# Kernel tuning notes

Measured on AMD Instinct MI355X. Metric: run time of the kernel, lower is better.

## Reference

```python
import jax, jax.numpy as jnp
import numpy as np

NUM_HEAD = 8  # matches init_kwargs num_head


def setup_inputs() -> dict:
    key = jax.random.key(0)
    ks = jax.random.split(key, 8)
    B, N, C, P = 2, 1024, 512, 256
    cluster_num = 8
    s = 0.02
    return {
        "x_token": jax.random.normal(ks[0], (B, N, C), jnp.float32),
        "x_path": jax.random.normal(ks[1], (B, N, P), jnp.float32),
        "idx_cluster": jax.random.randint(ks[2], (B, N), 0, cluster_num),
        "cluster_num": cluster_num,
        "Wq": jax.random.normal(ks[3], (C, C), jnp.float32) * s,
        "Wk": jax.random.normal(ks[4], (C, C), jnp.float32) * s,
        "Wv": jax.random.normal(ks[5], (C, C), jnp.float32) * s,
        "Wproj": jax.random.normal(ks[6], (C, C), jnp.float32) * s,
        "bproj": jnp.zeros((C,), jnp.float32),
    }


def reference(x_token, x_path, idx_cluster, cluster_num, Wq, Wk, Wv, Wproj, bproj):
    eps = 1e-6
    B, N, C = x_token.shape
    H = NUM_HEAD
    hd = C // H
    scale = hd ** -0.5

    # Linear projections (torch Linear: y = x @ W^T), qkv_bias=False
    q = x_token @ Wq.T
    k = x_token @ Wk.T
    v = (x_token @ Wv.T).reshape(B, N, H, hd).transpose(0, 2, 1, 3)  # (B,H,N,hd)

    qh = q.reshape(B, N, H, hd).transpose(0, 2, 1, 3)  # (B,H,N,hd)
    kh = k.reshape(B, N, H, hd).transpose(0, 2, 1, 3)

    # Raw scaled scores, computed once instead of per-cluster scatter/repeat
    s_ = jnp.einsum('bhid,bhjd->bhij', qh, kh) * scale  # (B,H,N,N)

    # One-hot cluster membership: (B, cluster_num, N)
    m = (idx_cluster[:, None, :] == jnp.arange(cluster_num)[None, :, None]).astype(s_.dtype)

    # attn_map[b,c,h,i,j] = s_[b,h,i,j] if idx[b,i]==c and idx[b,j]==c else 0
    attn_map = s_[:, None] * m[:, :, None, :, None] * m[:, :, None, None, :]  # (B,K,H,N,N)

    # Sum over clusters -> within-cluster scores, zeros elsewhere
    attn = attn_map.sum(axis=1)  # (B,H,N,N)

    # Custom eps-smoothed exp normalization (masked_fill on exact zeros, as in source)
    attn = jnp.where(attn == 0, jnp.float32(-1e9), attn).astype(jnp.float32)
    attn = jnp.exp(attn)
    attn = (attn + eps / N) / (attn.sum(axis=-1, keepdims=True) + eps)

    out = jnp.einsum('bhij,bhjd->bhid', attn, v)  # (B,H,N,hd)
    out = out.transpose(0, 2, 1, 3).reshape(B, N, C)
    out = out @ Wproj.T + bproj
    return out, attn_map
```

## Files before the change

### kernel.cpp

```cpp
#include <hip/hip_runtime.h>
#include <hip/hip_bf16.h>
#include <cstdint>
#include <cstddef>

#define NB   2
#define NN   1024
#define NC   512
#define NH   8
#define NHD  64
#define NK   8

typedef __attribute__((ext_vector_type(8))) short short8v;
typedef __attribute__((ext_vector_type(4))) short short4v;
typedef __attribute__((ext_vector_type(4))) float f32x4;

__device__ __forceinline__ short f2bf(float f) {
    union { float f; unsigned u; } v; v.f = f;
    unsigned r = v.u + 0x7FFFu + ((v.u >> 16) & 1u);
    return (short)(r >> 16);
}
__device__ __forceinline__ float bf2f(short s) {
    union { unsigned u; float f; } v;
    v.u = ((unsigned)(unsigned short)s) << 16;
    return v.f;
}
__device__ __forceinline__ short8v cvt8(const float* p) {
    float4 a = *(const float4*)p;
    float4 b = *(const float4*)(p + 4);
    short8v r;
    r[0] = f2bf(a.x); r[1] = f2bf(a.y); r[2] = f2bf(a.z); r[3] = f2bf(a.w);
    r[4] = f2bf(b.x); r[5] = f2bf(b.y); r[6] = f2bf(b.z); r[7] = f2bf(b.w);
    return r;
}

__global__ __launch_bounds__(256) void qkv_kernel(
    const float* __restrict__ x, const float* __restrict__ wq,
    const float* __restrict__ wk, const float* __restrict__ wv,
    short* __restrict__ qb, short* __restrict__ kb, short* __restrict__ vT) {
    __shared__ short As[64][40];
    __shared__ short Bs[64][40];
    const int tid = threadIdx.x;
    const int z = blockIdx.z;
    const float* Bsrc = (z == 0) ? wq : ((z == 1) ? wk : wv);
    const int m0 = blockIdx.y * 64, n0 = blockIdx.x * 64;
    const int lane = tid & 63, wave = tid >> 6;
    const int wm = wave >> 1, wn = wave & 1, quad = lane >> 4, lr = lane & 15;
    const int row = tid >> 2, c0 = (tid & 3) * 8;
    f32x4 acc[2][2] = {};
    for (int kt = 0; kt < 512; kt += 32) {
        *(short8v*)&As[row][c0] = cvt8(x + (m0 + row) * 512 + kt + c0);
        *(short8v*)&Bs[row][c0] = cvt8(Bsrc + (n0 + row) * 512 + kt + c0);
        __syncthreads();
        short8v a0 = *(short8v*)&As[wm * 32 + lr][quad * 8];
        short8v a1 = *(short8v*)&As[wm * 32 + 16 + lr][quad * 8];
        short8v b0 = *(short8v*)&Bs[wn * 32 + lr][quad * 8];
        short8v b1 = *(short8v*)&Bs[wn * 32 + 16 + lr][quad * 8];
        acc[0][0] = __builtin_amdgcn_mfma_f32_16x16x32_bf16(a0, b0, acc[0][0], 0, 0, 0);
        acc[0][1] = __builtin_amdgcn_mfma_f32_16x16x32_bf16(a0, b1, acc[0][1], 0, 0, 0);
        acc[1][0] = __builtin_amdgcn_mfma_f32_16x16x32_bf16(a1, b0, acc[1][0], 0, 0, 0);
        acc[1][1] = __builtin_amdgcn_mfma_f32_16x16x32_bf16(a1, b1, acc[1][1], 0, 0, 0);
        __syncthreads();
    }
    for (int sm = 0; sm < 2; sm++)
        for (int sn = 0; sn < 2; sn++)
            for (int r = 0; r < 4; r++) {
                int m = m0 + wm * 32 + sm * 16 + quad * 4 + r;
                int n = n0 + wn * 32 + sn * 16 + lr;
                short v = f2bf(acc[sm][sn][r]);
                if (z == 0) qb[m * 512 + n] = v;
                else if (z == 1) kb[m * 512 + n] = v;
                else {
                    int bb = m >> 10, i = m & 1023, h = n >> 6, d = n & 63;
                    vT[(size_t)(((bb * 8 + h) * 64 + d) << 10) + i] = v;
                }
            }
}

__global__ __launch_bounds__(256) void attn_fused_kernel(
    const short* __restrict__ qb, const short* __restrict__ kb,
    const short* __restrict__ vT, const int* __restrict__ idx,
    float* __restrict__ attn, short* __restrict__ oh) {
    __shared__ short Sm[16][1032];
    __shared__ short Qs[16][72], Ks[64][72], Vs[64][72], Es[16][72];
    __shared__ float Ss[16][68];
    __shared__ float rowpart[16][17];
    __shared__ float cpart[64][5];
    __shared__ float invL[16], csL[64];
    __shared__ int idxi[16], idxj[64];
    const int tid = threadIdx.x;
    const int z = blockIdx.y, b = z >> 3, h = z & 7;
    const int i0 = blockIdx.x * 16;
    const int lane = tid & 63, wave = tid >> 6;
    const int quad = lane >> 4, lr = lane & 15;
    const int r0 = tid >> 3, cc8 = (tid & 7) * 8;
    const int rL = tid >> 4, cI = tid & 15, cL = cI * 4;
    {
        int rq = tid >> 4, cq = (tid & 15) * 4;
        *(short4v*)&Qs[rq][cq] = *(const short4v*)(qb + (b * 1024 + i0 + rq) * 512 + h * 64 + cq);
    }
    if (tid < 16) idxi[tid] = idx[b * 1024 + i0 + tid];
    f32x4 acc_o = {};
    float rsum = 0.f;
    float csum = 0.f;
    for (int jt = 0; jt < 16; jt++) {
        const int j0 = jt * 64;
        *(short8v*)&Ks[r0][cc8]      = *(const short8v*)(kb + (b * 1024 + j0 + r0) * 512 + h * 64 + cc8);
        *(short8v*)&Ks[r0 + 32][cc8] = *(const short8v*)(kb + (b * 1024 + j0 + r0 + 32) * 512 + h * 64 + cc8);
        *(short8v*)&Vs[r0][cc8]      = *(const short8v*)(vT + ((size_t)z << 16) + (r0 << 10) + j0 + cc8);
        *(short8v*)&Vs[r0 + 32][cc8] = *(const short8v*)(vT + ((size_t)z << 16) + ((r0 + 32) << 10) + j0 + cc8);
        if (tid < 64) idxj[tid] = idx[b * 1024 + j0 + tid];
        __syncthreads();
        {
            const int d = tid >> 2, sg = (tid & 3) * 16;
            for (int u = 0; u < 16; u++) csum += bf2f(Vs[d][sg + u]);
        }
        f32x4 as = {};
        for (int k0 = 0; k0 < 64; k0 += 32) {
            short8v a0 = *(short8v*)&Qs[lr][k0 + quad * 8];
            short8v b0 = *(short8v*)&Ks[wave * 16 + lr][k0 + quad * 8];
            as = __builtin_amdgcn_mfma_f32_16x16x32_bf16(a0, b0, as, 0, 0, 0);
        }
        for (int r = 0; r < 4; r++)
            Ss[quad * 4 + r][wave * 16 + lr] = as[r] * 0.125f;
        __syncthreads();
        {
            const int ci = idxi[rL];
            f32x4 s4 = *(f32x4*)&Ss[rL][cL];
            short4v m4b, e4;
            for (int kk = 0; kk < 4; kk++) {
                const bool in = (idxj[cL + kk] == ci);
                const float sv = s4[kk];
                m4b[kk] = f2bf(in ? sv : 0.f);
                const float ev = (in && sv != 0.f) ? __expf(sv) : 0.f;
                rsum += ev;
                e4[kk] = f2bf(ev);
            }
            *(short4v*)&Sm[rL][j0 + cL] = m4b;
            *(short4v*)&Es[rL][cL] = e4;
        }
        __syncthreads();
        for (int k0 = 0; k0 < 64; k0 += 32) {
            short8v a0 = *(short8v*)&Es[lr][k0 + quad * 8];
            short8v b0 = *(short8v*)&Vs[wave * 16 + lr][k0 + quad * 8];
            acc_o = __builtin_amdgcn_mfma_f32_16x16x32_bf16(a0, b0, acc_o, 0, 0, 0);
        }
        __syncthreads();
    }
    rowpart[rL][cI] = rsum;
    cpart[tid >> 2][tid & 3] = csum;
    __syncthreads();
    if (tid < 16) {
        float v = 0.f;
        for (int s = 0; s < 16; s++) v += rowpart[tid][s];
        invL[tid] = 1.f / (v + 1e-6f);
    } else if (tid >= 64 && tid < 128) {
        const int d = tid - 64;
        csL[d] = cpart[d][0] + cpart[d][1] + cpart[d][2] + cpart[d][3];
    }
    __syncthreads();
    {
        const float epsN = 1e-6f / 1024.f;
        for (int r = 0; r < 4; r++) {
            int iLoc = quad * 4 + r;
            int d = wave * 16 + lr;
            float val = (acc_o[r] + epsN * csL[d]) * invL[iLoc];
            oh[((size_t)(b * 1024 + i0 + iLoc)) * 512 + h * 64 + d] = f2bf(val);
        }
    }
    const int tc = tid * 4;
    const f32x4 zv = {0.f, 0.f, 0.f, 0.f};
    for (int r = 0; r < 16; r++) {
        const int ci = idxi[r];
        short4v sm4 = *(short4v*)&Sm[r][tc];
        f32x4 mv;
        mv[0] = bf2f(sm4[0]); mv[1] = bf2f(sm4[1]);
        mv[2] = bf2f(sm4[2]); mv[3] = bf2f(sm4[3]);
        float* basebh = attn + (((size_t)(b * 64 + h)) << 20) + (((size_t)(i0 + r)) << 10) + tc;
        for (int c = 0; c < 8; c++) {
            f32x4 w = (c == ci) ? mv : zv;
            *(f32x4*)(basebh + ((size_t)c << 23)) = w;
        }
    }
}

__global__ __launch_bounds__(256) void proj_kernel(
    const short* __restrict__ oh, const float* __restrict__ wp,
    const float* __restrict__ bias, float* __restrict__ out) {
    __shared__ short As[64][40];
    __shared__ short Bs[64][40];
    const int tid = threadIdx.x;
    const int m0 = blockIdx.y * 64, n0 = blockIdx.x * 64;
    const int lane = tid & 63, wave = tid >> 6;
    const int wm = wave >> 1, wn = wave & 1, quad = lane >> 4, lr = lane & 15;
    const int row = tid >> 2, c0 = (tid & 3) * 8;
    f32x4 acc[2][2] = {};
    for (int kt = 0; kt < 512; kt += 32) {
        *(short8v*)&As[row][c0] = *(const short8v*)(oh + (m0 + row) * 512 + kt + c0);
        *(short8v*)&Bs[row][c0] = cvt8(wp + (n0 + row) * 512 + kt + c0);
        __syncthreads();
        short8v a0 = *(short8v*)&As[wm * 32 + lr][quad * 8];
        short8v a1 = *(short8v*)&As[wm * 32 + 16 + lr][quad * 8];
        short8v b0 = *(short8v*)&Bs[wn * 32 + lr][quad * 8];
        short8v b1 = *(short8v*)&Bs[wn * 32 + 16 + lr][quad * 8];
        acc[0][0] = __builtin_amdgcn_mfma_f32_16x16x32_bf16(a0, b0, acc[0][0], 0, 0, 0);
        acc[0][1] = __builtin_amdgcn_mfma_f32_16x16x32_bf16(a0, b1, acc[0][1], 0, 0, 0);
        acc[1][0] = __builtin_amdgcn_mfma_f32_16x16x32_bf16(a1, b0, acc[1][0], 0, 0, 0);
        acc[1][1] = __builtin_amdgcn_mfma_f32_16x16x32_bf16(a1, b1, acc[1][1], 0, 0, 0);
        __syncthreads();
    }
    for (int sm = 0; sm < 2; sm++)
        for (int sn = 0; sn < 2; sn++)
            for (int r = 0; r < 4; r++) {
                int m = m0 + wm * 32 + sm * 16 + quad * 4 + r;
                int n = n0 + wn * 32 + sn * 16 + lr;
                out[(size_t)m * 512 + n] = acc[sm][sn][r] + bias[n];
            }
}

extern "C" void kernel_launch(void* const* d_in, const int* in_sizes, int n_in,
                              void* d_out, int out_size, void* d_ws, size_t ws_size,
                              hipStream_t stream) {
    const float* x     = (const float*)d_in[0];
    const int*   idx   = (const int*)d_in[2];
    const float* Wq    = (const float*)d_in[4];
    const float* Wk    = (const float*)d_in[5];
    const float* Wv    = (const float*)d_in[6];
    const float* Wp    = (const float*)d_in[7];
    const float* bproj = (const float*)d_in[8];

    float* out  = (float*)d_out;
    float* attn = out + (size_t)NB * NN * NC;

    char* ws = (char*)d_ws;
    short* qb = (short*)(ws + 0);
    short* kb = (short*)(ws + 2097152);
    short* vT = (short*)(ws + 4194304);
    short* oh = (short*)(ws + 6291456);

    qkv_kernel<<<dim3(8, 32, 3), 256, 0, stream>>>(x, Wq, Wk, Wv, qb, kb, vT);
    attn_fused_kernel<<<dim3(64, 16), 256, 0, stream>>>(qb, kb, vT, idx, attn, oh);
    proj_kernel<<<dim3(8, 32, 1), 256, 0, stream>>>(oh, Wp, bproj, out);
}
```

Before: 618.7 us.

## Split zero-fill of attn_map into separate blocks and write cluster scores directly

Restructures the attention kernel grid into interleaved zero-fill blocks and compute blocks. Zero-fill blocks write zeros only for rows that belong to other clusters. Compute blocks write masked scores straight from the MFMA result into the owning cluster slice, which drops the Sm shared-memory staging and one barrier. The V column sums move into a separate small kernel so the inner loop no longer does that reduction. The goal is to spread the large 128MB attn_map store across many more blocks and cut per-block shared memory, at the cost of uncoalesced scalar stores from the compute path and an extra launch.

Measured after the change: 601.8 us. 2.7% less time.

```diff
diff --git a/kernel.cpp b/kernel.cpp
--- a/kernel.cpp
+++ b/kernel.cpp
@@ -76,32 +76,70 @@
             }
 }
 
+__global__ __launch_bounds__(256) void colsum_kernel(
+    const short* __restrict__ vT, float* __restrict__ colsum) {
+    __shared__ float cp[8][33];
+    const int blk = blockIdx.x;
+    const int bh = blk >> 3, dg = blk & 7;
+    const int t = threadIdx.x;
+    const int dl = t >> 5, seg = t & 31;
+    const short* p = vT + (((size_t)(bh * 64 + dg * 8 + dl)) << 10) + seg * 32;
+    float s = 0.f;
+    for (int k = 0; k < 32; k += 8) {
+        short8v v = *(const short8v*)(p + k);
+        for (int j = 0; j < 8; j++) s += bf2f(v[j]);
+    }
+    cp[dl][seg] = s;
+    __syncthreads();
+    if (t < 8) {
+        float v = 0.f;
+        for (int s2 = 0; s2 < 32; s2++) v += cp[t][s2];
+        colsum[bh * 64 + dg * 8 + t] = v;
+    }
+}
+
 __global__ __launch_bounds__(256) void attn_fused_kernel(
     const short* __restrict__ qb, const short* __restrict__ kb,
     const short* __restrict__ vT, const int* __restrict__ idx,
-    float* __restrict__ attn, short* __restrict__ oh) {
-    __shared__ short Sm[16][1032];
+    const float* __restrict__ colsum, float* __restrict__ attn,
+    short* __restrict__ oh) {
     __shared__ short Qs[16][72], Ks[64][72], Vs[64][72], Es[16][72];
-    __shared__ float Ss[16][68];
-    __shared__ float rowpart[16][17];
-    __shared__ float cpart[64][5];
+    __shared__ float rowpart[16][68];
     __shared__ float invL[16], csL[64];
-    __shared__ int idxi[16], idxj[64];
+    __shared__ int idxi[32], idxj[64];
     const int tid = threadIdx.x;
-    const int z = blockIdx.y, b = z >> 3, h = z & 7;
-    const int i0 = blockIdx.x * 16;
+    const int bi = blockIdx.x;
+    const int slot = bi % 5;
+
+    if (slot != 4) {
+        const int zb = (bi / 5) * 4 + slot;
+        const int itile = zb & 31, bch = zb >> 5;
+        const int c = (bch >> 3) & 7, b = bch >> 6;
+        if (tid < 32) idxi[tid] = idx[b * 1024 + itile * 32 + tid];
+        __syncthreads();
+        float* base = attn + ((size_t)bch << 20) + ((size_t)itile << 15);
+        const f32x4 zv = {0.f, 0.f, 0.f, 0.f};
+        for (int rr = 0; rr < 32; rr++) {
+            if (idxi[rr] == c) continue;
+            *(f32x4*)(base + (rr << 10) + tid * 4) = zv;
+        }
+        return;
+    }
+
+    const int vb = bi / 5;
+    const int z = vb >> 6, b = z >> 3, h = z & 7;
+    const int i0 = (vb & 63) * 16;
     const int lane = tid & 63, wave = tid >> 6;
     const int quad = lane >> 4, lr = lane & 15;
     const int r0 = tid >> 3, cc8 = (tid & 7) * 8;
-    const int rL = tid >> 4, cI = tid & 15, cL = cI * 4;
     {
         int rq = tid >> 4, cq = (tid & 15) * 4;
         *(short4v*)&Qs[rq][cq] = *(const short4v*)(qb + (b * 1024 + i0 + rq) * 512 + h * 64 + cq);
     }
     if (tid < 16) idxi[tid] = idx[b * 1024 + i0 + tid];
+    else if (tid >= 64 && tid < 128) csL[tid - 64] = colsum[z * 64 + (tid - 64)];
     f32x4 acc_o = {};
-    float rsum = 0.f;
-    float csum = 0.f;
+    float rsum[4] = {0.f, 0.f, 0.f, 0.f};
     for (int jt = 0; jt < 16; jt++) {
         const int j0 = jt * 64;
         *(short8v*)&Ks[r0][cc8]      = *(const short8v*)(kb + (b * 1024 + j0 + r0) * 512 + h * 64 + cc8);
@@ -110,33 +148,23 @@
         *(short8v*)&Vs[r0 + 32][cc8] = *(const short8v*)(vT + ((size_t)z << 16) + ((r0 + 32) << 10) + j0 + cc8);
         if (tid < 64) idxj[tid] = idx[b * 1024 + j0 + tid];
         __syncthreads();
-        {
-            const int d = tid >> 2, sg = (tid & 3) * 16;
-            for (int u = 0; u < 16; u++) csum += bf2f(Vs[d][sg + u]);
-        }
         f32x4 as = {};
         for (int k0 = 0; k0 < 64; k0 += 32) {
             short8v a0 = *(short8v*)&Qs[lr][k0 + quad * 8];
             short8v b0 = *(short8v*)&Ks[wave * 16 + lr][k0 + quad * 8];
             as = __builtin_amdgcn_mfma_f32_16x16x32_bf16(a0, b0, as, 0, 0, 0);
         }
-        for (int r = 0; r < 4; r++)
-            Ss[quad * 4 + r][wave * 16 + lr] = as[r] * 0.125f;
-        __syncthreads();
-        {
-            const int ci = idxi[rL];
-            f32x4 s4 = *(f32x4*)&Ss[rL][cL];
-            short4v m4b, e4;
-            for (int kk = 0; kk < 4; kk++) {
-                const bool in = (idxj[cL + kk] == ci);
-                const float sv = s4[kk];
-                m4b[kk] = f2bf(in ? sv : 0.f);
-                const float ev = (in && sv != 0.f) ? __expf(sv) : 0.f;
-                rsum += ev;
-                e4[kk] = f2bf(ev);
-            }
-            *(short4v*)&Sm[rL][j0 + cL] = m4b;
-            *(short4v*)&Es[rL][cL] = e4;
+        const int colc = idxj[wave * 16 + lr];
+        for (int r = 0; r < 4; r++) {
+            const int row = quad * 4 + r;
+            const int ci = idxi[row];
+            const float sv = as[r] * 0.125f;
+            const bool in = (colc == ci);
+            const float w = in ? sv : 0.f;
+            const float ev = (in && sv != 0.f) ? __expf(sv) : 0.f;
+            rsum[r] += ev;
+            Es[row][wave * 16 + lr] = f2bf(ev);
+            attn[(((size_t)(b * 64 + ci * 8 + h)) << 20) + (((size_t)(i0 + row)) << 10) + j0 + wave * 16 + lr] = w;
         }
         __syncthreads();
         for (int k0 = 0; k0 < 64; k0 += 32) {
@@ -146,40 +174,20 @@
         }
         __syncthreads();
     }
-    rowpart[rL][cI] = rsum;
-    cpart[tid >> 2][tid & 3] = csum;
+    for (int r = 0; r < 4; r++) rowpart[quad * 4 + r][wave * 16 + lr] = rsum[r];
     __syncthreads();
     if (tid < 16) {
         float v = 0.f;
-        for (int s = 0; s < 16; s++) v += rowpart[tid][s];
+        for (int s = 0; s < 64; s++) v += rowpart[tid][s];
         invL[tid] = 1.f / (v + 1e-6f);
-    } else if (tid >= 64 && tid < 128) {
-        const int d = tid - 64;
-        csL[d] = cpart[d][0] + cpart[d][1] + cpart[d][2] + cpart[d][3];
     }
     __syncthreads();
-    {
-        const float epsN = 1e-6f / 1024.f;
-        for (int r = 0; r < 4; r++) {
-            int iLoc = quad * 4 + r;
-            int d = wave * 16 + lr;
-            float val = (acc_o[r] + epsN * csL[d]) * invL[iLoc];
-            oh[((size_t)(b * 1024 + i0 + iLoc)) * 512 + h * 64 + d] = f2bf(val);
-        }
-    }
-    const int tc = tid * 4;
-    const f32x4 zv = {0.f, 0.f, 0.f, 0.f};
-    for (int r = 0; r < 16; r++) {
-        const int ci = idxi[r];
-        short4v sm4 = *(short4v*)&Sm[r][tc];
-        f32x4 mv;
-        mv[0] = bf2f(sm4[0]); mv[1] = bf2f(sm4[1]);
-        mv[2] = bf2f(sm4[2]); mv[3] = bf2f(sm4[3]);
-        float* basebh = attn + (((size_t)(b * 64 + h)) << 20) + (((size_t)(i0 + r)) << 10) + tc;
-        for (int c = 0; c < 8; c++) {
-            f32x4 w = (c == ci) ? mv : zv;
-            *(f32x4*)(basebh + ((size_t)c << 23)) = w;
-        }
+    const float epsN = 1e-6f / 1024.f;
+    for (int r = 0; r < 4; r++) {
+        const int row = quad * 4 + r;
+        const int d = wave * 16 + lr;
+        float val = (acc_o[r] + epsN * csL[d]) * invL[row];
+        oh[((size_t)(b * 1024 + i0 + row)) * 512 + h * 64 + d] = f2bf(val);
     }
 }
 
@@ -236,8 +244,10 @@
     short* kb = (short*)(ws + 2097152);
     short* vT = (short*)(ws + 4194304);
     short* oh = (short*)(ws + 6291456);
+    float* colsum = (float*)(ws + 8388608);
 
     qkv_kernel<<<dim3(8, 32, 3), 256, 0, stream>>>(x, Wq, Wk, Wv, qb, kb, vT);
-    attn_fused_kernel<<<dim3(64, 16), 256, 0, stream>>>(qb, kb, vT, idx, attn, oh);
+    colsum_kernel<<<128, 256, 0, stream>>>(vT, colsum);
+    attn_fused_kernel<<<5120, 256, 0, stream>>>(qb, kb, vT, idx, colsum, attn, oh);
     proj_kernel<<<dim3(8, 32, 1), 256, 0, stream>>>(oh, Wp, bproj, out);
 }
```
